# Kernel tuning notes

Hardware: AMD Instinct MI355X
Metric: run time of the kernel (lower is better)

## Reference

```python
import jax, jax.numpy as jnp
import numpy as np

N = 50000      # nodes (cells)
E = 800000     # directed edges
IN, H1, H2, Z = 512, 128, 128, 64


def setup_inputs() -> dict:
    key = jax.random.key(0)
    ks = jax.random.split(key, 12)
    x = jax.random.normal(ks[0], (N, IN), jnp.float32)
    edge_index = jax.random.randint(ks[1], (2, E), 0, N, dtype=jnp.int64)

    def glorot(k, i, o):
        return jax.random.normal(k, (i, o), jnp.float32) * np.float32(1.0 / np.sqrt(i))

    return {
        "x": x,
        "edge_index": edge_index,
        "W1": glorot(ks[2], IN, H1), "b1": jnp.zeros((H1,), jnp.float32),
        "W2": glorot(ks[3], H1, H2), "b2": jnp.zeros((H2,), jnp.float32),
        "Wm": glorot(ks[4], H2, Z),  "bm": jnp.zeros((Z,), jnp.float32),
        "Ws": glorot(ks[5], H2, Z),  "bs": jnp.zeros((Z,), jnp.float32),
    }


def _gcn_norm(edge_index, n):
    # PyG GCNConv default: add self-loops, sym-normalize D^-1/2 (A+I) D^-1/2
    loops = jnp.arange(n, dtype=edge_index.dtype)
    src = jnp.concatenate([edge_index[0], loops])
    dst = jnp.concatenate([edge_index[1], loops])
    deg = jax.ops.segment_sum(jnp.ones_like(dst, jnp.float32), dst, num_segments=n)
    dis = jnp.where(deg > 0, jax.lax.rsqrt(jnp.maximum(deg, 1.0)), 0.0)
    norm = dis[src] * dis[dst]  # [E+N]
    return src, dst, norm


def _gcn_conv(x, W, b, src, dst, norm, n):
    h = x @ W                          # [N, out] transform first
    msg = h[src] * norm[:, None]       # gather + scale
    out = jax.ops.segment_sum(msg, dst, num_segments=n)  # scatter-add at targets
    return out + b


def reference(x, edge_index, W1, b1, W2, b2, Wm, bm, Ws, bs):
    n = x.shape[0]
    src, dst, norm = _gcn_norm(edge_index, n)
    h = jax.nn.relu(_gcn_conv(x, W1, b1, src, dst, norm, n))
    h = jax.nn.relu(_gcn_conv(h, W2, b2, src, dst, norm, n))
    # dropout p=0.4 is identity in eval mode
    z_mean = _gcn_conv(h, Wm, bm, src, dst, norm, n)
    z_log_std = _gcn_conv(h, Ws, bs, src, dst, norm, n)
    return (z_mean, z_log_std)
```

## Files before the change

kernel.cpp:

```cpp
#include <hip/hip_runtime.h>


using u16 = unsigned short;
typedef __attribute__((ext_vector_type(8))) short short8;
typedef __attribute__((ext_vector_type(4))) float f32x4;

__device__ __forceinline__ void split_bf16(float f, u16& hi, u16& lo) {
    unsigned b = __float_as_uint(f);
    hi = (u16)(b >> 16);
    float rem = f - __uint_as_float(b & 0xFFFF0000u);
    lo = (u16)(__float_as_uint(rem) >> 16);
}

__device__ __forceinline__ int block_mode(const int* __restrict__ ew, int* sflag) {
    if (threadIdx.x == 0) *sflag = 0;
    __syncthreads();
    if (ew[2 * (int)threadIdx.x + 1] != 0) atomicOr(sflag, 1);
    __syncthreads();
    return *sflag ? 0 : 1;
}

__global__ void deg_kernel(const int* __restrict__ ew, int* __restrict__ deg, int E) {
    __shared__ int sflag;
    int mode = block_mode(ew, &sflag);
    int e = blockIdx.x * blockDim.x + threadIdx.x;
    if (e >= E) return;
    int d = mode ? ew[2 * E + 2 * e] : ew[E + e];
    atomicAdd(&deg[d], 1);
}

__global__ void scan_block_kernel(const int* __restrict__ deg, int* __restrict__ rowptr,
                                  int* __restrict__ aux, float* __restrict__ dis, int N) {
    __shared__ int s[256];
    int i = blockIdx.x * 256 + threadIdx.x;
    int v = (i < N) ? deg[i] : 0;
    if (i < N) dis[i] = rsqrtf((float)v + 1.0f);
    s[threadIdx.x] = v;
    __syncthreads();
    for (int off = 1; off < 256; off <<= 1) {
        int t = (threadIdx.x >= off) ? s[threadIdx.x - off] : 0;
        __syncthreads();
        s[threadIdx.x] += t;
        __syncthreads();
    }
    if (i < N) rowptr[i] = s[threadIdx.x] - v;
    if (threadIdx.x == 255) aux[blockIdx.x] = s[255];
}

__global__ void scan_aux_kernel(int* __restrict__ aux, int nb) {
    __shared__ int s[256];
    int i = threadIdx.x;
    int v = (i < nb) ? aux[i] : 0;
    s[i] = v;
    __syncthreads();
    for (int off = 1; off < 256; off <<= 1) {
        int t = (i >= off) ? s[i - off] : 0;
        __syncthreads();
        s[i] += t;
        __syncthreads();
    }
    if (i < nb) aux[i] = s[i] - v;
}

__global__ void add_offsets_kernel(int* __restrict__ rowptr, const int* __restrict__ aux,
                                   int N, int E) {
    int i = blockIdx.x * 256 + threadIdx.x;
    if (i < N) rowptr[i] += aux[i >> 8];
    if (i == 0) rowptr[N] = E;
}

__global__ void fill_csr_kernel(const int* __restrict__ ew,
                                const int* __restrict__ rowptr, int* __restrict__ cursor,
                                int* __restrict__ csr_src, int E) {
    __shared__ int sflag;
    int mode = block_mode(ew, &sflag);
    int e = blockIdx.x * blockDim.x + threadIdx.x;
    if (e >= E) return;
    int s = mode ? ew[2 * e] : ew[e];
    int d = mode ? ew[2 * E + 2 * e] : ew[E + e];
    int pos = rowptr[d] + atomicAdd(&cursor[d], 1);
    csr_src[pos] = s;
}

__global__ void conv_all_kernel(const float* __restrict__ W1, const float* __restrict__ W2,
                                const float* __restrict__ Wm, const float* __restrict__ Ws,
                                u16* __restrict__ W1t_hi, u16* __restrict__ W1t_lo,
                                u16* __restrict__ W2t_hi, u16* __restrict__ W2t_lo,
                                u16* __restrict__ Wct_hi, u16* __restrict__ Wct_lo) {
    int idx = blockIdx.x * 256 + threadIdx.x;
    u16 h, l;
    if (idx < 65536) {
        int k = idx >> 7, n = idx & 127;
        split_bf16(W1[idx], h, l);
        W1t_hi[n * 512 + k] = h;
        W1t_lo[n * 512 + k] = l;
    } else if (idx < 81920) {
        int t = idx - 65536;
        int k = t >> 7, n = t & 127;
        split_bf16(W2[t], h, l);
        W2t_hi[n * 128 + k] = h;
        W2t_lo[n * 128 + k] = l;
    } else if (idx < 98304) {
        int t = idx - 81920;
        int k = t >> 7, j = t & 127;
        float f = (j < 64) ? Wm[k * 64 + j] : Ws[k * 64 + (j - 64)];
        split_bf16(f, h, l);
        Wct_hi[j * 128 + k] = h;
        Wct_lo[j * 128 + k] = l;
    }
}

template <int K, bool SPLIT>
__global__ __launch_bounds__(256) void gemm_direct(
    const float* __restrict__ A,
    const u16* __restrict__ Ahi, const u16* __restrict__ Alo,
    const u16* __restrict__ Bh, const u16* __restrict__ Bl,
    float* __restrict__ C, int N) {
    const int tid = threadIdx.x;
    const int w = tid >> 6, lane = tid & 63;
    const int row0 = blockIdx.x * 64;
    const int R = (w >> 1) * 32, Cc = (w & 1) * 64;
    const int m16 = lane & 15, quad = lane >> 4, kq = quad * 8;

    int r0 = row0 + R + m16;
    int r1 = r0 + 16;
    if (r0 > N - 1) r0 = N - 1;
    if (r1 > N - 1) r1 = N - 1;

    const float* a0;
    const float* a1;
    const u16 *ah0, *ah1, *al0, *al1;
    if constexpr (SPLIT) {
        ah0 = Ahi + (size_t)r0 * K + kq;
        ah1 = Ahi + (size_t)r1 * K + kq;
        al0 = Alo + (size_t)r0 * K + kq;
        al1 = Alo + (size_t)r1 * K + kq;
    } else {
        a0 = A + (size_t)r0 * K + kq;
        a1 = A + (size_t)r1 * K + kq;
    }
    const u16* bhp[4];
    const u16* blp[4];
#pragma unroll
    for (int j = 0; j < 4; ++j) {
        int n = Cc + j * 16 + m16;
        bhp[j] = Bh + (size_t)n * K + kq;
        blp[j] = Bl + (size_t)n * K + kq;
    }

    f32x4 acc[2][4];
#pragma unroll
    for (int i = 0; i < 2; ++i)
#pragma unroll
        for (int j = 0; j < 4; ++j) acc[i][j] = (f32x4)0.f;

    float curA[2][8];
    short8 curAh[2], curAl[2];
    short8 curBh[4], curBl[4];

    if constexpr (SPLIT) {
        curAh[0] = *(const short8*)&ah0[0];
        curAh[1] = *(const short8*)&ah1[0];
        curAl[0] = *(const short8*)&al0[0];
        curAl[1] = *(const short8*)&al1[0];
    } else {
        f32x4 v00 = *(const f32x4*)&a0[0], v01 = *(const f32x4*)&a0[4];
        f32x4 v10 = *(const f32x4*)&a1[0], v11 = *(const f32x4*)&a1[4];
#pragma unroll
        for (int q = 0; q < 4; ++q) {
            curA[0][q] = v00[q]; curA[0][4 + q] = v01[q];
            curA[1][q] = v10[q]; curA[1][4 + q] = v11[q];
        }
    }
#pragma unroll
    for (int j = 0; j < 4; ++j) {
        curBh[j] = *(const short8*)&bhp[j][0];
        curBl[j] = *(const short8*)&blp[j][0];
    }

    const int NSTEP = K / 32;
#pragma unroll
    for (int ks = 0; ks < NSTEP; ++ks) {
        float nxtA[2][8];
        short8 nxtAh[2], nxtAl[2], nxtBh[4], nxtBl[4];
        const bool more = (ks + 1 < NSTEP);
        if (more) {
            const int kb = (ks + 1) * 32;
            if constexpr (SPLIT) {
                nxtAh[0] = *(const short8*)&ah0[kb];
                nxtAh[1] = *(const short8*)&ah1[kb];
                nxtAl[0] = *(const short8*)&al0[kb];
                nxtAl[1] = *(const short8*)&al1[kb];
            } else {
                f32x4 v00 = *(const f32x4*)&a0[kb], v01 = *(const f32x4*)&a0[kb + 4];
                f32x4 v10 = *(const f32x4*)&a1[kb], v11 = *(const f32x4*)&a1[kb + 4];
#pragma unroll
                for (int q = 0; q < 4; ++q) {
                    nxtA[0][q] = v00[q]; nxtA[0][4 + q] = v01[q];
                    nxtA[1][q] = v10[q]; nxtA[1][4 + q] = v11[q];
                }
            }
#pragma unroll
            for (int j = 0; j < 4; ++j) {
                nxtBh[j] = *(const short8*)&bhp[j][kb];
                nxtBl[j] = *(const short8*)&blp[j][kb];
            }
        }

        short8 ah[2], al[2];
        if constexpr (SPLIT) {
#pragma unroll
            for (int i = 0; i < 2; ++i) { ah[i] = curAh[i]; al[i] = curAl[i]; }
        } else {
#pragma unroll
            for (int i = 0; i < 2; ++i)
#pragma unroll
                for (int q = 0; q < 8; ++q) {
                    u16 h, l;
                    split_bf16(curA[i][q], h, l);
                    ah[i][q] = (short)h;
                    al[i][q] = (short)l;
                }
        }

#pragma unroll
        for (int i = 0; i < 2; ++i)
#pragma unroll
            for (int j = 0; j < 4; ++j) {
                acc[i][j] = __builtin_amdgcn_mfma_f32_16x16x32_bf16(
                    ah[i], curBh[j], acc[i][j], 0, 0, 0);
                acc[i][j] = __builtin_amdgcn_mfma_f32_16x16x32_bf16(
                    ah[i], curBl[j], acc[i][j], 0, 0, 0);
                acc[i][j] = __builtin_amdgcn_mfma_f32_16x16x32_bf16(
                    al[i], curBh[j], acc[i][j], 0, 0, 0);
            }

        if (more) {
            if constexpr (SPLIT) {
#pragma unroll
                for (int i = 0; i < 2; ++i) { curAh[i] = nxtAh[i]; curAl[i] = nxtAl[i]; }
            } else {
#pragma unroll
                for (int i = 0; i < 2; ++i)
#pragma unroll
                    for (int q = 0; q < 8; ++q) curA[i][q] = nxtA[i][q];
            }
#pragma unroll
            for (int j = 0; j < 4; ++j) { curBh[j] = nxtBh[j]; curBl[j] = nxtBl[j]; }
        }
    }

#pragma unroll
    for (int i = 0; i < 2; ++i) {
#pragma unroll
        for (int r = 0; r < 4; ++r) {
            int gr = row0 + R + i * 16 + quad * 4 + r;
            if (gr < N) {
#pragma unroll
                for (int j = 0; j < 4; ++j)
                    C[(size_t)gr * 128 + Cc + j * 16 + m16] = acc[i][j][r];
            }
        }
    }
}

__global__ __launch_bounds__(256) void propagate_kernel(
    const float* __restrict__ h, const int* __restrict__ rowptr,
    const int* __restrict__ csr_src, const float* __restrict__ dis,
    const float* __restrict__ bias, u16* __restrict__ out_hi,
    u16* __restrict__ out_lo, int N) {
    int wave = (blockIdx.x * 256 + threadIdx.x) >> 6;
    int lane = threadIdx.x & 63;
    if (wave >= N) return;
    int v = wave;
    int f = lane * 2;
    float dv = dis[v];
    float ax = 0.f, ay = 0.f;
    int beg = rowptr[v], end = rowptr[v + 1];
    int i = beg;
    for (; i + 8 <= end; i += 8) {
        int s[8];
        float ww[8];
        float2 g[8];
#pragma unroll
        for (int u = 0; u < 8; ++u) s[u] = csr_src[i + u];
#pragma unroll
        for (int u = 0; u < 8; ++u) ww[u] = dis[s[u]];
#pragma unroll
        for (int u = 0; u < 8; ++u) g[u] = *(const float2*)&h[(size_t)s[u] * 128 + f];
#pragma unroll
        for (int u = 0; u < 8; ++u) {
            float t = ww[u] * dv;
            ax += t * g[u].x;
            ay += t * g[u].y;
        }
    }
    if (i + 4 <= end) {
        int s[4];
        float ww[4];
        float2 g[4];
#pragma unroll
        for (int u = 0; u < 4; ++u) s[u] = csr_src[i + u];
#pragma unroll
        for (int u = 0; u < 4; ++u) ww[u] = dis[s[u]];
#pragma unroll
        for (int u = 0; u < 4; ++u) g[u] = *(const float2*)&h[(size_t)s[u] * 128 + f];
#pragma unroll
        for (int u = 0; u < 4; ++u) {
            float t = ww[u] * dv;
            ax += t * g[u].x;
            ay += t * g[u].y;
        }
        i += 4;
    }
    for (; i < end; ++i) {
        int s = csr_src[i];
        float ws = dis[s] * dv;
        float2 g = *(const float2*)&h[(size_t)s * 128 + f];
        ax += ws * g.x;
        ay += ws * g.y;
    }
    float2 hv = *(const float2*)&h[(size_t)v * 128 + f];
    ax += dv * dv * hv.x;
    ay += dv * dv * hv.y;
    ax += bias[f];
    ay += bias[f + 1];
    ax = fmaxf(ax, 0.f);
    ay = fmaxf(ay, 0.f);
    u16 hx, lx, hy, ly;
    split_bf16(ax, hx, lx);
    split_bf16(ay, hy, ly);
    *(ushort2*)&out_hi[(size_t)v * 128 + f] = make_ushort2(hx, hy);
    *(ushort2*)&out_lo[(size_t)v * 128 + f] = make_ushort2(lx, ly);
}

__global__ __launch_bounds__(256) void propagate_final_kernel(
    const float* __restrict__ h, const int* __restrict__ rowptr,
    const int* __restrict__ csr_src, const float* __restrict__ dis,
    const float* __restrict__ bm, const float* __restrict__ bs,
    float* __restrict__ out, int N) {
    int wave = (blockIdx.x * 256 + threadIdx.x) >> 6;
    int lane = threadIdx.x & 63;
    if (wave >= N) return;
    int v = wave;
    int f = lane * 2;
    float dv = dis[v];
    float ax = 0.f, ay = 0.f;
    int beg = rowptr[v], end = rowptr[v + 1];
    int i = beg;
    for (; i + 8 <= end; i += 8) {
        int s[8];
        float ww[8];
        float2 g[8];
#pragma unroll
        for (int u = 0; u < 8; ++u) s[u] = csr_src[i + u];
#pragma unroll
        for (int u = 0; u < 8; ++u) ww[u] = dis[s[u]];
#pragma unroll
        for (int u = 0; u < 8; ++u) g[u] = *(const float2*)&h[(size_t)s[u] * 128 + f];
#pragma unroll
        for (int u = 0; u < 8; ++u) {
            float t = ww[u] * dv;
            ax += t * g[u].x;
            ay += t * g[u].y;
        }
    }
    if (i + 4 <= end) {
        int s[4];
        float ww[4];
        float2 g[4];
#pragma unroll
        for (int u = 0; u < 4; ++u) s[u] = csr_src[i + u];
#pragma unroll
        for (int u = 0; u < 4; ++u) ww[u] = dis[s[u]];
#pragma unroll
        for (int u = 0; u < 4; ++u) g[u] = *(const float2*)&h[(size_t)s[u] * 128 + f];
#pragma unroll
        for (int u = 0; u < 4; ++u) {
            float t = ww[u] * dv;
            ax += t * g[u].x;
            ay += t * g[u].y;
        }
        i += 4;
    }
    for (; i < end; ++i) {
        int s = csr_src[i];
        float ws = dis[s] * dv;
        float2 g = *(const float2*)&h[(size_t)s * 128 + f];
        ax += ws * g.x;
        ay += ws * g.y;
    }
    float2 hv = *(const float2*)&h[(size_t)v * 128 + f];
    ax += dv * dv * hv.x;
    ay += dv * dv * hv.y;
    if (f < 64) {
        *(float2*)&out[(size_t)v * 64 + f] = make_float2(ax + bm[f], ay + bm[f + 1]);
    } else {
        int g = f - 64;
        *(float2*)&out[(size_t)N * 64 + (size_t)v * 64 + g] =
            make_float2(ax + bs[g], ay + bs[g + 1]);
    }
}

extern "C" void kernel_launch(void* const* d_in, const int* in_sizes, int n_in,
                              void* d_out, int out_size, void* d_ws, size_t ws_size,
                              hipStream_t stream) {
    const float* x  = (const float*)d_in[0];
    const int*   ew = (const int*)d_in[1];
    const float* W1 = (const float*)d_in[2];
    const float* b1 = (const float*)d_in[3];
    const float* W2 = (const float*)d_in[4];
    const float* b2 = (const float*)d_in[5];
    const float* Wm = (const float*)d_in[6];
    const float* bm = (const float*)d_in[7];
    const float* Ws = (const float*)d_in[8];
    const float* bs = (const float*)d_in[9];
    float* out = (float*)d_out;

    const int IN = 512, H = 128;
    const int N = in_sizes[0] / IN;
    const int E = in_sizes[1] / 2;

    char* base = (char*)d_ws;
    size_t off = 0;
    auto alloc = [&](size_t bytes) -> char* {
        char* p = base + off;
        off = (off + bytes + 255) & ~(size_t)255;
        return p;
    };
    char*  degcur  = (char*) alloc(400384);
    float* dis     = (float*)alloc((size_t)N * 4);
    int*   rowptr  = (int*)  alloc((size_t)(N + 1) * 4);
    int*   aux     = (int*)  alloc(256 * 4);
    int*   csr_src = (int*)  alloc((size_t)E * 4);
    u16*   W1t_hi  = (u16*)  alloc((size_t)IN * H * 2);
    u16*   W1t_lo  = (u16*)  alloc((size_t)IN * H * 2);
    u16*   W2t_hi  = (u16*)  alloc((size_t)H * H * 2);
    u16*   W2t_lo  = (u16*)  alloc((size_t)H * H * 2);
    u16*   Wct_hi  = (u16*)  alloc((size_t)H * H * 2);
    u16*   Wct_lo  = (u16*)  alloc((size_t)H * H * 2);
    float* hA      = (float*)alloc((size_t)N * H * 4);
    u16*   hBhi    = (u16*)  alloc((size_t)N * H * 2);
    u16*   hBlo    = (u16*)  alloc((size_t)N * H * 2);
    (void)ws_size; (void)n_in; (void)out_size;

    int* deg    = (int*)degcur;
    int* cursor = (int*)(degcur + 200192);

    hipMemsetAsync(degcur, 0, 400384, stream);

    const int eblocks = (E + 255) / 256;
    const int nblocks = (N + 255) / 256;

    conv_all_kernel<<<(98304 + 255) / 256, 256, 0, stream>>>(
        W1, W2, Wm, Ws, W1t_hi, W1t_lo, W2t_hi, W2t_lo, Wct_hi, Wct_lo);
    deg_kernel<<<eblocks, 256, 0, stream>>>(ew, deg, E);
    scan_block_kernel<<<nblocks, 256, 0, stream>>>(deg, rowptr, aux, dis, N);
    scan_aux_kernel<<<1, 256, 0, stream>>>(aux, nblocks);
    add_offsets_kernel<<<nblocks, 256, 0, stream>>>(rowptr, aux, N, E);
    fill_csr_kernel<<<eblocks, 256, 0, stream>>>(ew, rowptr, cursor, csr_src, E);

    const int gblocks = (N + 63) / 64;
    const int pblocks = (N * 64 + 255) / 256;

    gemm_direct<512, false><<<gblocks, 256, 0, stream>>>(
        x, nullptr, nullptr, W1t_hi, W1t_lo, hA, N);
    propagate_kernel<<<pblocks, 256, 0, stream>>>(hA, rowptr, csr_src, dis,
                                                  b1, hBhi, hBlo, N);
    gemm_direct<128, true><<<gblocks, 256, 0, stream>>>(
        nullptr, hBhi, hBlo, W2t_hi, W2t_lo, hA, N);
    propagate_kernel<<<pblocks, 256, 0, stream>>>(hA, rowptr, csr_src, dis,
                                                  b2, hBhi, hBlo, N);
    gemm_direct<128, true><<<gblocks, 256, 0, stream>>>(
        nullptr, hBhi, hBlo, Wct_hi, Wct_lo, hA, N);
    propagate_final_kernel<<<pblocks, 256, 0, stream>>>(hA, rowptr, csr_src, dis,
                                                        bm, bs, out, N);
}
```

Before: 561.2 us.

## Stage GEMM operands through shared memory and merge weight-conversion with degree kernel

Replaces the direct-from-global MFMA GEMM with a version that loads A and B tiles cooperatively into padded LDS buffers, so each operand element is fetched from global once per block instead of once per wave. Block row tile shrinks from 64 to 32 rows, giving each wave one A fragment and four B fragments. The fp32-to-bf16 split of A is now done once per element rather than redundantly across waves. Separately, the weight-conversion and degree-count kernels are fused into one launch to save a kernel launch, at the cost of two barriers per k-step and twice as many B reloads across blocks.

```diff
diff --git a/kernel.cpp b/kernel.cpp
--- a/kernel.cpp
+++ b/kernel.cpp
@@ -20,13 +20,43 @@
     return *sflag ? 0 : 1;
 }
 
-__global__ void deg_kernel(const int* __restrict__ ew, int* __restrict__ deg, int E) {
-    __shared__ int sflag;
-    int mode = block_mode(ew, &sflag);
-    int e = blockIdx.x * blockDim.x + threadIdx.x;
-    if (e >= E) return;
-    int d = mode ? ew[2 * E + 2 * e] : ew[E + e];
-    atomicAdd(&deg[d], 1);
+#define CONVB 384
+__global__ void conv_deg_kernel(const float* __restrict__ W1, const float* __restrict__ W2,
+                                const float* __restrict__ Wm, const float* __restrict__ Ws,
+                                u16* __restrict__ W1t_hi, u16* __restrict__ W1t_lo,
+                                u16* __restrict__ W2t_hi, u16* __restrict__ W2t_lo,
+                                u16* __restrict__ Wct_hi, u16* __restrict__ Wct_lo,
+                                const int* __restrict__ ew, int* __restrict__ deg, int E) {
+    if (blockIdx.x < CONVB) {
+        int idx = blockIdx.x * 256 + threadIdx.x;
+        u16 h, l;
+        if (idx < 65536) {
+            int k = idx >> 7, n = idx & 127;
+            split_bf16(W1[idx], h, l);
+            W1t_hi[n * 512 + k] = h;
+            W1t_lo[n * 512 + k] = l;
+        } else if (idx < 81920) {
+            int t = idx - 65536;
+            int k = t >> 7, n = t & 127;
+            split_bf16(W2[t], h, l);
+            W2t_hi[n * 128 + k] = h;
+            W2t_lo[n * 128 + k] = l;
+        } else if (idx < 98304) {
+            int t = idx - 81920;
+            int k = t >> 7, j = t & 127;
+            float f = (j < 64) ? Wm[k * 64 + j] : Ws[k * 64 + (j - 64)];
+            split_bf16(f, h, l);
+            Wct_hi[j * 128 + k] = h;
+            Wct_lo[j * 128 + k] = l;
+        }
+    } else {
+        __shared__ int sflag;
+        int mode = block_mode(ew, &sflag);
+        int e = (blockIdx.x - CONVB) * 256 + threadIdx.x;
+        if (e >= E) return;
+        int d = mode ? ew[2 * E + 2 * e] : ew[E + e];
+        atomicAdd(&deg[d], 1);
+    }
 }
 
 __global__ void scan_block_kernel(const int* __restrict__ deg, int* __restrict__ rowptr,
@@ -82,184 +112,127 @@
     csr_src[pos] = s;
 }
 
-__global__ void conv_all_kernel(const float* __restrict__ W1, const float* __restrict__ W2,
-                                const float* __restrict__ Wm, const float* __restrict__ Ws,
-                                u16* __restrict__ W1t_hi, u16* __restrict__ W1t_lo,
-                                u16* __restrict__ W2t_hi, u16* __restrict__ W2t_lo,
-                                u16* __restrict__ Wct_hi, u16* __restrict__ Wct_lo) {
-    int idx = blockIdx.x * 256 + threadIdx.x;
-    u16 h, l;
-    if (idx < 65536) {
-        int k = idx >> 7, n = idx & 127;
-        split_bf16(W1[idx], h, l);
-        W1t_hi[n * 512 + k] = h;
-        W1t_lo[n * 512 + k] = l;
-    } else if (idx < 81920) {
-        int t = idx - 65536;
-        int k = t >> 7, n = t & 127;
-        split_bf16(W2[t], h, l);
-        W2t_hi[n * 128 + k] = h;
-        W2t_lo[n * 128 + k] = l;
-    } else if (idx < 98304) {
-        int t = idx - 81920;
-        int k = t >> 7, j = t & 127;
-        float f = (j < 64) ? Wm[k * 64 + j] : Ws[k * 64 + (j - 64)];
-        split_bf16(f, h, l);
-        Wct_hi[j * 128 + k] = h;
-        Wct_lo[j * 128 + k] = l;
-    }
-}
+#define TILE_OFF(t) ((t) * 520)
 
 template <int K, bool SPLIT>
-__global__ __launch_bounds__(256) void gemm_direct(
+__global__ __launch_bounds__(256) void gemm_tiled(
     const float* __restrict__ A,
     const u16* __restrict__ Ahi, const u16* __restrict__ Alo,
     const u16* __restrict__ Bh, const u16* __restrict__ Bl,
     float* __restrict__ C, int N) {
+    __shared__ u16 AsH[2 * 520], AsL[2 * 520];
+    __shared__ u16 BsH[8 * 520], BsL[8 * 520];
+
     const int tid = threadIdx.x;
+    const int row0 = blockIdx.x * 32;
+
+    const int arow = tid >> 3;
+    const int akq  = (tid & 7) * 4;
+    const int a_dst = TILE_OFF(arow >> 4) + ((arow & 15) + 16 * (akq >> 3)) * 8 + (akq & 7);
+    const int s_bc = tid >> 1;
+    const int s_bk = (tid & 1) * 16;
+    const int b_q0 = (tid & 1) * 2;
+    const int b_dst0 = TILE_OFF(s_bc >> 4) + ((s_bc & 15) + 16 * (b_q0 + 0)) * 8;
+    const int b_dst1 = TILE_OFF(s_bc >> 4) + ((s_bc & 15) + 16 * (b_q0 + 1)) * 8;
+
     const int w = tid >> 6, lane = tid & 63;
-    const int row0 = blockIdx.x * 64;
-    const int R = (w >> 1) * 32, Cc = (w & 1) * 64;
-    const int m16 = lane & 15, quad = lane >> 4, kq = quad * 8;
-
-    int r0 = row0 + R + m16;
-    int r1 = r0 + 16;
-    if (r0 > N - 1) r0 = N - 1;
-    if (r1 > N - 1) r1 = N - 1;
-
-    const float* a0;
-    const float* a1;
-    const u16 *ah0, *ah1, *al0, *al1;
+    const int aw = w >> 1;
+    const int Cc = (w & 1) * 64;
+    const int btile = (w & 1) * 4;
+    const int m16 = lane & 15, quad = lane >> 4;
+
+    f32x4 acc[4];
+#pragma unroll
+    for (int j = 0; j < 4; ++j) acc[j] = (f32x4)0.f;
+
+    int gr = row0 + arow;
+    if (gr > N - 1) gr = N - 1;
+    const float* ap;
+    const u16 *ahp, *alp;
     if constexpr (SPLIT) {
-        ah0 = Ahi + (size_t)r0 * K + kq;
-        ah1 = Ahi + (size_t)r1 * K + kq;
-        al0 = Alo + (size_t)r0 * K + kq;
-        al1 = Alo + (size_t)r1 * K + kq;
+        ahp = Ahi + (size_t)gr * K + akq;
+        alp = Alo + (size_t)gr * K + akq;
     } else {
-        a0 = A + (size_t)r0 * K + kq;
-        a1 = A + (size_t)r1 * K + kq;
-    }
-    const u16* bhp[4];
-    const u16* blp[4];
-#pragma unroll
-    for (int j = 0; j < 4; ++j) {
-        int n = Cc + j * 16 + m16;
-        bhp[j] = Bh + (size_t)n * K + kq;
-        blp[j] = Bl + (size_t)n * K + kq;
-    }
-
-    f32x4 acc[2][4];
-#pragma unroll
-    for (int i = 0; i < 2; ++i)
-#pragma unroll
-        for (int j = 0; j < 4; ++j) acc[i][j] = (f32x4)0.f;
-
-    float curA[2][8];
-    short8 curAh[2], curAl[2];
-    short8 curBh[4], curBl[4];
-
+        ap = A + (size_t)gr * K + akq;
+    }
+    const u16* bph = Bh + (size_t)s_bc * K + s_bk;
+    const u16* bpl = Bl + (size_t)s_bc * K + s_bk;
+
+    f32x4 avc;
+    ushort4 ahc, alc;
+    short8 bh0, bh1, bl0, bl1;
     if constexpr (SPLIT) {
-        curAh[0] = *(const short8*)&ah0[0];
-        curAh[1] = *(const short8*)&ah1[0];
-        curAl[0] = *(const short8*)&al0[0];
-        curAl[1] = *(const short8*)&al1[0];
+        ahc = *(const ushort4*)&ahp[0];
+        alc = *(const ushort4*)&alp[0];
     } else {
-        f32x4 v00 = *(const f32x4*)&a0[0], v01 = *(const f32x4*)&a0[4];
-        f32x4 v10 = *(const f32x4*)&a1[0], v11 = *(const f32x4*)&a1[4];
-#pragma unroll
-        for (int q = 0; q < 4; ++q) {
-            curA[0][q] = v00[q]; curA[0][4 + q] = v01[q];
-            curA[1][q] = v10[q]; curA[1][4 + q] = v11[q];
-        }
-    }
-#pragma unroll
-    for (int j = 0; j < 4; ++j) {
-        curBh[j] = *(const short8*)&bhp[j][0];
-        curBl[j] = *(const short8*)&blp[j][0];
-    }
+        avc = *(const f32x4*)&ap[0];
+    }
+    bh0 = *(const short8*)&bph[0];
+    bh1 = *(const short8*)&bph[8];
+    bl0 = *(const short8*)&bpl[0];
+    bl1 = *(const short8*)&bpl[8];
 
     const int NSTEP = K / 32;
 #pragma unroll
     for (int ks = 0; ks < NSTEP; ++ks) {
-        float nxtA[2][8];
-        short8 nxtAh[2], nxtAl[2], nxtBh[4], nxtBl[4];
-        const bool more = (ks + 1 < NSTEP);
-        if (more) {
+        ushort4 wh, wl;
+        if constexpr (SPLIT) {
+            wh = ahc; wl = alc;
+        } else {
+#pragma unroll
+            for (int q = 0; q < 4; ++q) {
+                u16 h, l;
+                split_bf16(avc[q], h, l);
+                (&wh.x)[q] = h;
+                (&wl.x)[q] = l;
+            }
+        }
+        __syncthreads();
+        *(ushort4*)&AsH[a_dst] = wh;
+        *(ushort4*)&AsL[a_dst] = wl;
+        *(short8*)&BsH[b_dst0] = bh0;
+        *(short8*)&BsH[b_dst1] = bh1;
+        *(short8*)&BsL[b_dst0] = bl0;
+        *(short8*)&BsL[b_dst1] = bl1;
+        __syncthreads();
+
+        if (ks + 1 < NSTEP) {
             const int kb = (ks + 1) * 32;
             if constexpr (SPLIT) {
-                nxtAh[0] = *(const short8*)&ah0[kb];
-                nxtAh[1] = *(const short8*)&ah1[kb];
-                nxtAl[0] = *(const short8*)&al0[kb];
-                nxtAl[1] = *(const short8*)&al1[kb];
+                ahc = *(const ushort4*)&ahp[kb];
+                alc = *(const ushort4*)&alp[kb];
             } else {
-                f32x4 v00 = *(const f32x4*)&a0[kb], v01 = *(const f32x4*)&a0[kb + 4];
-                f32x4 v10 = *(const f32x4*)&a1[kb], v11 = *(const f32x4*)&a1[kb + 4];
-#pragma unroll
-                for (int q = 0; q < 4; ++q) {
-                    nxtA[0][q] = v00[q]; nxtA[0][4 + q] = v01[q];
-                    nxtA[1][q] = v10[q]; nxtA[1][4 + q] = v11[q];
-                }
+                avc = *(const f32x4*)&ap[kb];
             }
-#pragma unroll
-            for (int j = 0; j < 4; ++j) {
-                nxtBh[j] = *(const short8*)&bhp[j][kb];
-                nxtBl[j] = *(const short8*)&blp[j][kb];
-            }
-        }
-
-        short8 ah[2], al[2];
-        if constexpr (SPLIT) {
-#pragma unroll
-            for (int i = 0; i < 2; ++i) { ah[i] = curAh[i]; al[i] = curAl[i]; }
-        } else {
-#pragma unroll
-            for (int i = 0; i < 2; ++i)
-#pragma unroll
-                for (int q = 0; q < 8; ++q) {
-                    u16 h, l;
-                    split_bf16(curA[i][q], h, l);
-                    ah[i][q] = (short)h;
-                    al[i][q] = (short)l;
-                }
-        }
-
-#pragma unroll
-        for (int i = 0; i < 2; ++i)
-#pragma unroll
-            for (int j = 0; j < 4; ++j) {
-                acc[i][j] = __builtin_amdgcn_mfma_f32_16x16x32_bf16(
-                    ah[i], curBh[j], acc[i][j], 0, 0, 0);
-                acc[i][j] = __builtin_amdgcn_mfma_f32_16x16x32_bf16(
-                    ah[i], curBl[j], acc[i][j], 0, 0, 0);
-                acc[i][j] = __builtin_amdgcn_mfma_f32_16x16x32_bf16(
-                    al[i], curBh[j], acc[i][j], 0, 0, 0);
-            }
-
-        if (more) {
-            if constexpr (SPLIT) {
-#pragma unroll
-                for (int i = 0; i < 2; ++i) { curAh[i] = nxtAh[i]; curAl[i] = nxtAl[i]; }
-            } else {
-#pragma unroll
-                for (int i = 0; i < 2; ++i)
-#pragma unroll
-                    for (int q = 0; q < 8; ++q) curA[i][q] = nxtA[i][q];
-            }
-#pragma unroll
-            for (int j = 0; j < 4; ++j) { curBh[j] = nxtBh[j]; curBl[j] = nxtBl[j]; }
-        }
-    }
-
-#pragma unroll
-    for (int i = 0; i < 2; ++i) {
-#pragma unroll
-        for (int r = 0; r < 4; ++r) {
-            int gr = row0 + R + i * 16 + quad * 4 + r;
-            if (gr < N) {
-#pragma unroll
-                for (int j = 0; j < 4; ++j)
-                    C[(size_t)gr * 128 + Cc + j * 16 + m16] = acc[i][j][r];
-            }
+            bh0 = *(const short8*)&bph[kb];
+            bh1 = *(const short8*)&bph[kb + 8];
+            bl0 = *(const short8*)&bpl[kb];
+            bl1 = *(const short8*)&bpl[kb + 8];
+        }
+
+        short8 fa_h = *(const short8*)&AsH[TILE_OFF(aw) + lane * 8];
+        short8 fa_l = *(const short8*)&AsL[TILE_OFF(aw) + lane * 8];
+        short8 fb_h[4], fb_l[4];
+#pragma unroll
+        for (int j = 0; j < 4; ++j) {
+            fb_h[j] = *(const short8*)&BsH[TILE_OFF(btile + j) + lane * 8];
+            fb_l[j] = *(const short8*)&BsL[TILE_OFF(btile + j) + lane * 8];
+        }
+#pragma unroll
+        for (int j = 0; j < 4; ++j) {
+            acc[j] = __builtin_amdgcn_mfma_f32_16x16x32_bf16(fa_h, fb_h[j], acc[j], 0, 0, 0);
+            acc[j] = __builtin_amdgcn_mfma_f32_16x16x32_bf16(fa_h, fb_l[j], acc[j], 0, 0, 0);
+            acc[j] = __builtin_amdgcn_mfma_f32_16x16x32_bf16(fa_l, fb_h[j], acc[j], 0, 0, 0);
+        }
+    }
+
+#pragma unroll
+    for (int r = 0; r < 4; ++r) {
+        int grr = row0 + aw * 16 + quad * 4 + r;
+        if (grr < N) {
+#pragma unroll
+            for (int j = 0; j < 4; ++j)
+                C[(size_t)grr * 128 + Cc + j * 16 + m16] = acc[j][r];
         }
     }
 }
@@ -452,26 +425,26 @@
     const int eblocks = (E + 255) / 256;
     const int nblocks = (N + 255) / 256;
 
-    conv_all_kernel<<<(98304 + 255) / 256, 256, 0, stream>>>(
-        W1, W2, Wm, Ws, W1t_hi, W1t_lo, W2t_hi, W2t_lo, Wct_hi, Wct_lo);
-    deg_kernel<<<eblocks, 256, 0, stream>>>(ew, deg, E);
+    conv_deg_kernel<<<CONVB + eblocks, 256, 0, stream>>>(
+        W1, W2, Wm, Ws, W1t_hi, W1t_lo, W2t_hi, W2t_lo, Wct_hi, Wct_lo,
+        ew, deg, E);
     scan_block_kernel<<<nblocks, 256, 0, stream>>>(deg, rowptr, aux, dis, N);
     scan_aux_kernel<<<1, 256, 0, stream>>>(aux, nblocks);
     add_offsets_kernel<<<nblocks, 256, 0, stream>>>(rowptr, aux, N, E);
     fill_csr_kernel<<<eblocks, 256, 0, stream>>>(ew, rowptr, cursor, csr_src, E);
 
-    const int gblocks = (N + 63) / 64;
+    const int gblocks = (N + 31) / 32;
     const int pblocks = (N * 64 + 255) / 256;
 
-    gemm_direct<512, false><<<gblocks, 256, 0, stream>>>(
+    gemm_tiled<512, false><<<gblocks, 256, 0, stream>>>(
         x, nullptr, nullptr, W1t_hi, W1t_lo, hA, N);
     propagate_kernel<<<pblocks, 256, 0, stream>>>(hA, rowptr, csr_src, dis,
                                                   b1, hBhi, hBlo, N);
-    gemm_direct<128, true><<<gblocks, 256, 0, stream>>>(
+    gemm_tiled<128, true><<<gblocks, 256, 0, stream>>>(
         nullptr, hBhi, hBlo, W2t_hi, W2t_lo, hA, N);
     propagate_kernel<<<pblocks, 256, 0, stream>>>(hA, rowptr, csr_src, dis,
                                                   b2, hBhi, hBlo, N);
-    gemm_direct<128, true><<<gblocks, 256, 0, stream>>>(
+    gemm_tiled<128, true><<<gblocks, 256, 0, stream>>>(
         nullptr, hBhi, hBlo, Wct_hi, Wct_lo, hA, N);
     propagate_final_kernel<<<pblocks, 256, 0, stream>>>(hA, rowptr, csr_src, dis,
                                                         bm, bs, out, N);
```

Result: faster. 515.0 us (-8.2%).
